# Kernel optimization log

Measured on AMD Instinct MI355X. Metric: run time of the kernel, lower is better.

Reference implementation:

```python
import jax, jax.numpy as jnp
from jax import lax
import numpy as np

PAD = 1          # padding (pair, symmetric)
STRIDE = (1, 1)  # (strideY, strideX)
KH, KW = 3, 3
C_IN, C_OUT = 256, 512


def setup_inputs() -> dict:
    key = jax.random.key(0)
    k1, k2 = jax.random.split(key)
    x = jax.random.normal(k1, (1, C_IN, 256, 256), dtype=jnp.float32)
    # reset_parameters: uniform(-stdv, stdv), stdv = 1/sqrt(numel(weight))
    stdv = 1.0 / np.sqrt(C_OUT * C_IN * KH * KW)
    weight = jax.random.uniform(k2, (C_OUT, C_IN, KH, KW), dtype=jnp.float32,
                                minval=-stdv, maxval=stdv)
    return {"x": x, "weight": weight}


def reference(x, weight):
    # pad H and W with constant value 1 (as in module's pad())
    xp = jnp.pad(x, ((0, 0), (0, 0), (PAD, PAD), (PAD, PAD)), constant_values=1.0)
    # binarize input: (x >= 0) -> +1 else -1 (detached in torch; non-diff anyway)
    xb = jnp.where(xp >= 0, 1.0, -1.0).astype(x.dtype)
    # input_K: channel-mean of |x| then avg_pool2d(kernel, stride), VALID
    abs_mean = jnp.mean(jnp.abs(xp), axis=1)  # [B, Hp, Wp]
    k_sum = lax.reduce_window(abs_mean, 0.0, lax.add,
                              (1, KH, KW), (1,) + STRIDE, 'VALID')
    input_K = k_sum / (KH * KW)  # [B, Ho, Wo]
    # binary conv (real-valued emulation of XNOR+popcount)
    conv = lax.conv_general_dilated(xb, weight, window_strides=STRIDE,
                                    padding='VALID',
                                    dimension_numbers=('NCHW', 'OIHW', 'NCHW'))
    # weight_alpha: per-output-channel mean of weight (note: mean, not abs-mean,
    # in the training-path forward())
    alpha = jnp.mean(weight, axis=(1, 2, 3))  # [C_out]
    return conv * input_K[:, None, :, :] * alpha[None, :, None, None]
```

## Files before the change

kernel.cpp:

```cpp
#include <hip/hip_runtime.h>

typedef unsigned short UST;
typedef unsigned int u32;
typedef __attribute__((ext_vector_type(4))) int i32x4;

#define HPAD 258
#define CIN 256
#define COUT 512
#define KTOT 2304

#define SCALES_OFF (COUT * KTOT)
#define XBT_OFF    (SCALES_OFF + 2048)
#define XBT_BYTES  (HPAD * HPAD * CIN)
#define ABSM_OFF   (XBT_OFF + XBT_BYTES)
#define ABSM_BYTES (HPAD * HPAD * 4)
#define INK_OFF    (ABSM_OFF + ABSM_BYTES)

__device__ __forceinline__ void gload_lds16(const void* g, void* l) {
  __builtin_amdgcn_global_load_lds(
      (const __attribute__((address_space(1))) u32*)g,
      (__attribute__((address_space(3))) u32*)l, 16, 0, 0);
}

__global__ __launch_bounds__(256) void k_prep_w(const float* __restrict__ w,
                                                signed char* __restrict__ wq,
                                                float* __restrict__ scales) {
  int co = blockIdx.x;
  int ci = threadIdx.x;
  const float* wr = w + co * KTOT + ci * 9;
  float v[9];
  float s = 0.f, mx = 0.f;
#pragma unroll
  for (int j = 0; j < 9; ++j) {
    v[j] = wr[j]; s += v[j]; mx = fmaxf(mx, fabsf(v[j]));
  }
  __shared__ float redS[256];
  __shared__ float redM[256];
  redS[ci] = s; redM[ci] = mx;
  __syncthreads();
#pragma unroll
  for (int off = 128; off > 0; off >>= 1) {
    if (ci < off) {
      redS[ci] += redS[ci + off];
      redM[ci] = fmaxf(redM[ci], redM[ci + off]);
    }
    __syncthreads();
  }
  float alpha = redS[0] * (1.0f / 2304.0f);
  float maxw = redM[0];
  float inv = 127.0f / maxw;
  signed char* wo = wq + co * KTOT + ci;
#pragma unroll
  for (int j = 0; j < 9; ++j)
    wo[j * 256] = (signed char)__float2int_rn(v[j] * inv);
  if (ci == 0) scales[co] = alpha * maxw * (1.0f / 127.0f);
}

__global__ __launch_bounds__(256) void k_binz(const float* __restrict__ x,
                                              signed char* __restrict__ xbt,
                                              float* __restrict__ absm) {
  int hp = blockIdx.x;
  int wt = blockIdx.y;
  int wpl = threadIdx.x & 63;
  int chunk = threadIdx.x >> 6;
  int wp = wt * 64 + wpl;
  bool valid = wp < HPAD;
  int hx = hp - 1, wx = wp - 1;
  bool inb = valid && ((unsigned)hx < 256u) && ((unsigned)wx < 256u);
  float asum = 0.f;
  u32 pk[16];
#pragma unroll
  for (int c4 = 0; c4 < 16; ++c4) {
    u32 word = 0;
#pragma unroll
    for (int b = 0; b < 4; ++b) {
      int ci = chunk * 64 + c4 * 4 + b;
      float v = 1.0f;
      if (inb) v = x[(unsigned)ci * 65536u + (unsigned)(hx * 256 + wx)];
      asum += fabsf(v);
      u32 byte = (v >= 0.f) ? 0x01u : 0xFFu;
      word |= byte << (8 * b);
    }
    pk[c4] = word;
  }
  if (valid) {
    uint4* dst = (uint4*)(xbt + (unsigned)(hp * HPAD + wp) * 256u + chunk * 64);
#pragma unroll
    for (int g = 0; g < 4; ++g)
      dst[g] = make_uint4(pk[g * 4], pk[g * 4 + 1], pk[g * 4 + 2], pk[g * 4 + 3]);
  }
  __shared__ float red[4][64];
  red[chunk][wpl] = asum;
  __syncthreads();
  if (chunk == 0 && valid) {
    float tot = red[0][wpl] + red[1][wpl] + red[2][wpl] + red[3][wpl];
    absm[hp * HPAD + wp] = tot * (1.0f / 256.0f);
  }
}

__global__ __launch_bounds__(256) void k_inputk(const float* __restrict__ absm,
                                                float* __restrict__ inK) {
  int h = blockIdx.x, w = threadIdx.x;
  float s = 0.f;
#pragma unroll
  for (int dh = 0; dh < 3; ++dh)
#pragma unroll
    for (int dw = 0; dw < 3; ++dw) s += absm[(h + dh) * HPAD + (w + dw)];
  inK[h * 256 + w] = s * (1.0f / 9.0f);
}

#define MMI(a, b, c) __builtin_amdgcn_mfma_i32_16x16x64_i8(a, b, c, 0, 0, 0)

#define A_LDS(S) (lds + (S) * 32768)
#define B_LDS(S) (lds + 65536 + (S) * 32768)
#define RD_A(S, KS, M) (*(const i32x4*)(A_LDS(S) + swzA[KS][M]))
#define RD_B(S, KS, N) (*(const i32x4*)(B_LDS(S) + swzB[KS][N]))

#define STAGE_A(SRC, S) do { \
    char* d_ = A_LDS(S) + wv * 1024; \
    gload_lds16((SRC) + aoff[0], d_); \
    gload_lds16((SRC) + aoff[1], d_ + 8192); \
    gload_lds16((SRC) + aoff[2], d_ + 16384); \
    gload_lds16((SRC) + aoff[3], d_ + 24576); } while (0)

#define STAGE_B(SRC, S) do { \
    char* d_ = B_LDS(S) + wv * 1024; \
    gload_lds16((SRC) + boff[0], d_); \
    gload_lds16((SRC) + boff[1], d_ + 8192); \
    gload_lds16((SRC) + boff[2], d_ + 16384); \
    gload_lds16((SRC) + boff[3], d_ + 24576); } while (0)

#define SB __builtin_amdgcn_sched_barrier(0)
#define VMW(N) asm volatile("s_waitcnt vmcnt(" #N ")" ::: "memory")
#define LGK0 asm volatile("s_waitcnt lgkmcnt(0)" ::: "memory")

#define RDB4(S, KS, D) \
  D[0] = RD_B(S, KS, 0); D[1] = RD_B(S, KS, 1); \
  D[2] = RD_B(S, KS, 2); D[3] = RD_B(S, KS, 3);
#define RDALO(S, KS, D) \
  D[0] = RD_A(S, KS, 0); D[1] = RD_A(S, KS, 1); \
  D[2] = RD_A(S, KS, 2); D[3] = RD_A(S, KS, 3);
#define RDAHI(S, KS, D) \
  D[0] = RD_A(S, KS, 4); D[1] = RD_A(S, KS, 5); \
  D[2] = RD_A(S, KS, 6); D[3] = RD_A(S, KS, 7);

#define MF_LO(AA, BB) \
  __builtin_amdgcn_s_setprio(1); \
  _Pragma("unroll") for (int m = 0; m < 4; ++m) \
  _Pragma("unroll") for (int n = 0; n < 4; ++n) \
    acc[m][n] = MMI(AA[m], BB[n], acc[m][n]); \
  __builtin_amdgcn_s_setprio(0);
#define MF_HI(AA, BB) \
  __builtin_amdgcn_s_setprio(1); \
  _Pragma("unroll") for (int m = 0; m < 4; ++m) \
  _Pragma("unroll") for (int n = 0; n < 4; ++n) \
    acc[m + 4][n] = MMI(AA[m], BB[n], acc[m + 4][n]); \
  __builtin_amdgcn_s_setprio(0);

#define BGPX(TT) (xbt_b + ((h + ((TT) >> 1) / 3) * HPAD + (((TT) >> 1) % 3)) * 256 \
                  + ((TT) & 1) * 128)

#define BODY(CA, CB, SA, SBT, TA, TB, ASRC, BSRC) do { \
  i32x4 Ahi_[4], B1_[4], A1lo_[4], A1hi_[4]; \
  RDAHI(CA, 0, Ahi_); \
  STAGE_A((ASRC), SA); STAGE_B((BSRC), SBT); \
  SB; MF_LO(Alo_, B0_); SB; \
  RDB4(CB, 1, B1_); RDALO(CA, 1, A1lo_); \
  SB; MF_HI(Ahi_, B0_); SB; \
  RDAHI(CA, 1, A1hi_); \
  SB; MF_LO(A1lo_, B1_); SB; \
  LGK0; VMW(4); \
  __builtin_amdgcn_s_barrier(); \
  RDB4(TB, 0, B0_); RDALO(TA, 0, Alo_); \
  SB; MF_HI(A1hi_, B1_); SB; \
} while (0)

#define BU(U) BODY((U) & 1, (U) % 3, ((U) + 1) & 1, ((U) + 2) % 3, \
                   ((U) + 1) & 1, ((U) + 1) % 3, \
                   wb_b + ((U) + 1) * 128, BGPX((U) + 2))

#define BODY16() do { \
  i32x4 Ahi_[4], B1_[4], A1lo_[4], A1hi_[4]; \
  RDAHI(0, 0, Ahi_); \
  STAGE_A(wb_b + 17 * 128, 1); \
  SB; MF_LO(Alo_, B0_); SB; \
  RDB4(1, 1, B1_); RDALO(0, 1, A1lo_); \
  SB; MF_HI(Ahi_, B0_); SB; \
  RDAHI(0, 1, A1hi_); \
  SB; MF_LO(A1lo_, B1_); SB; \
  LGK0; VMW(0); \
  __builtin_amdgcn_s_barrier(); \
  RDB4(2, 0, B0_); RDALO(1, 0, Alo_); \
  SB; MF_HI(A1hi_, B1_); SB; \
} while (0)

#define BODY17() do { \
  i32x4 Ahi_[4], B1_[4], A1lo_[4], A1hi_[4]; \
  RDAHI(1, 0, Ahi_); \
  SB; MF_LO(Alo_, B0_); SB; \
  RDB4(2, 1, B1_); RDALO(1, 1, A1lo_); \
  SB; MF_HI(Ahi_, B0_); SB; \
  RDAHI(1, 1, A1hi_); \
  SB; MF_LO(A1lo_, B1_); SB; \
  SB; MF_HI(A1hi_, B1_); SB; \
} while (0)

__global__ __launch_bounds__(512, 1) void k_conv8(const signed char* __restrict__ wq,
                                                  const signed char* __restrict__ xbt,
                                                  const float* __restrict__ scales,
                                                  const float* __restrict__ inK,
                                                  float* __restrict__ out) {
  __shared__ __align__(16) char lds[163840];
  int tid = threadIdx.x;
  int lane = tid & 63;
  int wv = tid >> 6;
  int wm = wv >> 2, wn = wv & 3;
  int bid = blockIdx.x;
  int bs = (bid & 7) * 64 + (bid >> 3);
  int mt = bs & 1;
  int h = bs >> 1;
  int co0 = mt << 8;

  int aoff[4], boff[4];
#pragma unroll
  for (int i = 0; i < 4; ++i) {
    u32 ql = (u32)(i * 512 + tid) * 16u;
    u32 row = ql >> 7;
    u32 s = (ql >> 4) & 7u;
    u32 slot = s ^ (row & 7u);
    aoff[i] = (int)((co0 + row) * 2304u + slot * 16u);
    boff[i] = (int)(row * 256u + slot * 16u);
  }
  int swzA[2][8], swzB[2][4];
#pragma unroll
  for (int ks = 0; ks < 2; ++ks) {
#pragma unroll
    for (int m = 0; m < 8; ++m) {
      u32 row = (u32)(wm * 128 + m * 16 + (lane & 15));
      u32 slot = (u32)(ks * 4 + (lane >> 4));
      swzA[ks][m] = (int)(row * 128u + (slot ^ (row & 7u)) * 16u);
    }
#pragma unroll
    for (int n = 0; n < 4; ++n) {
      u32 row = (u32)(wn * 64 + n * 16 + (lane & 15));
      u32 slot = (u32)(ks * 4 + (lane >> 4));
      swzB[ks][n] = (int)(row * 128u + (slot ^ (row & 7u)) * 16u);
    }
  }

  const char* wb_b = (const char*)wq;
  const char* xbt_b = (const char*)xbt;

  i32x4 acc[8][4];
#pragma unroll
  for (int m = 0; m < 8; ++m)
#pragma unroll
    for (int n = 0; n < 4; ++n) acc[m][n] = (i32x4){0, 0, 0, 0};

  i32x4 B0_[4], Alo_[4];

  STAGE_A(wb_b, 0);
  STAGE_B(BGPX(0), 0);
  STAGE_B(BGPX(1), 1);
  VMW(4);
  __builtin_amdgcn_s_barrier();
  RDB4(0, 0, B0_); RDALO(0, 0, Alo_);

  BU(0); BU(1); BU(2); BU(3); BU(4); BU(5); BU(6); BU(7);
  BU(8); BU(9); BU(10); BU(11); BU(12); BU(13); BU(14); BU(15);
  BODY16();
  BODY17();

  int col = lane & 15, rg = lane >> 4;
  int pixbase = h * 256;
#pragma unroll
  for (int n = 0; n < 4; ++n) {
    int w = wn * 64 + n * 16 + col;
    float kv = inK[pixbase + w];
#pragma unroll
    for (int m = 0; m < 8; ++m) {
      int cobase = co0 + wm * 128 + m * 16 + rg * 4;
      float4 scv = *(const float4*)(scales + cobase);
      float* o = out + (u32)cobase * 65536u + (u32)(pixbase + w);
      o[0]           = (float)acc[m][n][0] * scv.x * kv;
      o[65536u]      = (float)acc[m][n][1] * scv.y * kv;
      o[2u * 65536u] = (float)acc[m][n][2] * scv.z * kv;
      o[3u * 65536u] = (float)acc[m][n][3] * scv.w * kv;
    }
  }
}

extern "C" void kernel_launch(void* const* d_in, const int* in_sizes, int n_in,
                              void* d_out, int out_size, void* d_ws, size_t ws_size,
                              hipStream_t stream) {
  const float* x = (const float*)d_in[0];
  const float* w = (const float*)d_in[1];
  float* out = (float*)d_out;
  char* ws = (char*)d_ws;
  signed char* wq = (signed char*)ws;
  float* scales = (float*)(ws + SCALES_OFF);
  signed char* xbt = (signed char*)(ws + XBT_OFF);
  float* absm = (float*)(ws + ABSM_OFF);
  float* inK = (float*)(ws + INK_OFF);

  k_prep_w<<<COUT, 256, 0, stream>>>(w, wq, scales);
  k_binz<<<dim3(HPAD, 5), 256, 0, stream>>>(x, xbt, absm);
  k_inputk<<<256, 256, 0, stream>>>(absm, inK);
  k_conv8<<<512, 512, 0, stream>>>(wq, xbt, scales, inK, out);
}
```

Before: 108.6 us.

## Merge prep kernels into one launch, fold inputK into conv epilogue, hoist Ahi reads

```diff
diff --git a/kernel.cpp b/kernel.cpp
--- a/kernel.cpp
+++ b/kernel.cpp
@@ -13,8 +13,6 @@
 #define XBT_OFF    (SCALES_OFF + 2048)
 #define XBT_BYTES  (HPAD * HPAD * CIN)
 #define ABSM_OFF   (XBT_OFF + XBT_BYTES)
-#define ABSM_BYTES (HPAD * HPAD * 4)
-#define INK_OFF    (ABSM_OFF + ABSM_BYTES)
 
 __device__ __forceinline__ void gload_lds16(const void* g, void* l) {
   __builtin_amdgcn_global_load_lds(
@@ -22,91 +20,83 @@
       (__attribute__((address_space(3))) u32*)l, 16, 0, 0);
 }
 
-__global__ __launch_bounds__(256) void k_prep_w(const float* __restrict__ w,
-                                                signed char* __restrict__ wq,
-                                                float* __restrict__ scales) {
-  int co = blockIdx.x;
-  int ci = threadIdx.x;
-  const float* wr = w + co * KTOT + ci * 9;
-  float v[9];
-  float s = 0.f, mx = 0.f;
-#pragma unroll
-  for (int j = 0; j < 9; ++j) {
-    v[j] = wr[j]; s += v[j]; mx = fmaxf(mx, fabsf(v[j]));
-  }
-  __shared__ float redS[256];
-  __shared__ float redM[256];
-  redS[ci] = s; redM[ci] = mx;
-  __syncthreads();
-#pragma unroll
-  for (int off = 128; off > 0; off >>= 1) {
-    if (ci < off) {
-      redS[ci] += redS[ci + off];
-      redM[ci] = fmaxf(redM[ci], redM[ci + off]);
-    }
-    __syncthreads();
-  }
-  float alpha = redS[0] * (1.0f / 2304.0f);
-  float maxw = redM[0];
-  float inv = 127.0f / maxw;
-  signed char* wo = wq + co * KTOT + ci;
-#pragma unroll
-  for (int j = 0; j < 9; ++j)
-    wo[j * 256] = (signed char)__float2int_rn(v[j] * inv);
-  if (ci == 0) scales[co] = alpha * maxw * (1.0f / 127.0f);
-}
-
-__global__ __launch_bounds__(256) void k_binz(const float* __restrict__ x,
+__global__ __launch_bounds__(256) void k_prep(const float* __restrict__ w,
+                                              signed char* __restrict__ wq,
+                                              float* __restrict__ scales,
+                                              const float* __restrict__ x,
                                               signed char* __restrict__ xbt,
                                               float* __restrict__ absm) {
-  int hp = blockIdx.x;
-  int wt = blockIdx.y;
-  int wpl = threadIdx.x & 63;
-  int chunk = threadIdx.x >> 6;
-  int wp = wt * 64 + wpl;
-  bool valid = wp < HPAD;
-  int hx = hp - 1, wx = wp - 1;
-  bool inb = valid && ((unsigned)hx < 256u) && ((unsigned)wx < 256u);
-  float asum = 0.f;
-  u32 pk[16];
-#pragma unroll
-  for (int c4 = 0; c4 < 16; ++c4) {
-    u32 word = 0;
-#pragma unroll
-    for (int b = 0; b < 4; ++b) {
-      int ci = chunk * 64 + c4 * 4 + b;
-      float v = 1.0f;
-      if (inb) v = x[(unsigned)ci * 65536u + (unsigned)(hx * 256 + wx)];
-      asum += fabsf(v);
-      u32 byte = (v >= 0.f) ? 0x01u : 0xFFu;
-      word |= byte << (8 * b);
-    }
-    pk[c4] = word;
-  }
-  if (valid) {
-    uint4* dst = (uint4*)(xbt + (unsigned)(hp * HPAD + wp) * 256u + chunk * 64);
-#pragma unroll
-    for (int g = 0; g < 4; ++g)
-      dst[g] = make_uint4(pk[g * 4], pk[g * 4 + 1], pk[g * 4 + 2], pk[g * 4 + 3]);
-  }
-  __shared__ float red[4][64];
-  red[chunk][wpl] = asum;
-  __syncthreads();
-  if (chunk == 0 && valid) {
-    float tot = red[0][wpl] + red[1][wpl] + red[2][wpl] + red[3][wpl];
-    absm[hp * HPAD + wp] = tot * (1.0f / 256.0f);
-  }
-}
-
-__global__ __launch_bounds__(256) void k_inputk(const float* __restrict__ absm,
-                                                float* __restrict__ inK) {
-  int h = blockIdx.x, w = threadIdx.x;
-  float s = 0.f;
-#pragma unroll
-  for (int dh = 0; dh < 3; ++dh)
-#pragma unroll
-    for (int dw = 0; dw < 3; ++dw) s += absm[(h + dh) * HPAD + (w + dw)];
-  inK[h * 256 + w] = s * (1.0f / 9.0f);
+  int bid = blockIdx.x;
+  if (bid < COUT) {
+    int co = bid;
+    int ci = threadIdx.x;
+    const float* wr = w + co * KTOT + ci * 9;
+    float v[9];
+    float s = 0.f, mx = 0.f;
+#pragma unroll
+    for (int j = 0; j < 9; ++j) {
+      v[j] = wr[j]; s += v[j]; mx = fmaxf(mx, fabsf(v[j]));
+    }
+    __shared__ float redS[256];
+    __shared__ float redM[256];
+    redS[ci] = s; redM[ci] = mx;
+    __syncthreads();
+#pragma unroll
+    for (int off = 128; off > 0; off >>= 1) {
+      if (ci < off) {
+        redS[ci] += redS[ci + off];
+        redM[ci] = fmaxf(redM[ci], redM[ci + off]);
+      }
+      __syncthreads();
+    }
+    float alpha = redS[0] * (1.0f / 2304.0f);
+    float maxw = redM[0];
+    float inv = 127.0f / maxw;
+    signed char* wo = wq + co * KTOT + ci;
+#pragma unroll
+    for (int j = 0; j < 9; ++j)
+      wo[j * 256] = (signed char)__float2int_rn(v[j] * inv);
+    if (ci == 0) scales[co] = alpha * maxw * (1.0f / 127.0f);
+  } else {
+    int b2 = bid - COUT;
+    int hp = b2 / 5;
+    int wt = b2 - hp * 5;
+    int wpl = threadIdx.x & 63;
+    int chunk = threadIdx.x >> 6;
+    int wp = wt * 64 + wpl;
+    bool valid = wp < HPAD;
+    int hx = hp - 1, wx = wp - 1;
+    bool inb = valid && ((unsigned)hx < 256u) && ((unsigned)wx < 256u);
+    float asum = 0.f;
+    u32 pk[16];
+#pragma unroll
+    for (int c4 = 0; c4 < 16; ++c4) {
+      u32 word = 0;
+#pragma unroll
+      for (int b = 0; b < 4; ++b) {
+        int ci = chunk * 64 + c4 * 4 + b;
+        float v = 1.0f;
+        if (inb) v = x[(unsigned)ci * 65536u + (unsigned)(hx * 256 + wx)];
+        asum += fabsf(v);
+        u32 byte = (v >= 0.f) ? 0x01u : 0xFFu;
+        word |= byte << (8 * b);
+      }
+      pk[c4] = word;
+    }
+    if (valid) {
+      uint4* dst = (uint4*)(xbt + (unsigned)(hp * HPAD + wp) * 256u + chunk * 64);
+#pragma unroll
+      for (int g = 0; g < 4; ++g)
+        dst[g] = make_uint4(pk[g * 4], pk[g * 4 + 1], pk[g * 4 + 2], pk[g * 4 + 3]);
+    }
+    __shared__ float red[4][64];
+    red[chunk][wpl] = asum;
+    __syncthreads();
+    if (chunk == 0 && valid) {
+      float tot = red[0][wpl] + red[1][wpl] + red[2][wpl] + red[3][wpl];
+      absm[hp * HPAD + wp] = tot * (1.0f / 256.0f);
+    }
+  }
 }
 
 #define MMI(a, b, c) __builtin_amdgcn_mfma_i32_16x16x64_i8(a, b, c, 0, 0, 0)
@@ -161,8 +151,7 @@
                   + ((TT) & 1) * 128)
 
 #define BODY(CA, CB, SA, SBT, TA, TB, ASRC, BSRC) do { \
-  i32x4 Ahi_[4], B1_[4], A1lo_[4], A1hi_[4]; \
-  RDAHI(CA, 0, Ahi_); \
+  i32x4 B1_[4], A1lo_[4], A1hi_[4]; \
   STAGE_A((ASRC), SA); STAGE_B((BSRC), SBT); \
   SB; MF_LO(Alo_, B0_); SB; \
   RDB4(CB, 1, B1_); RDALO(CA, 1, A1lo_); \
@@ -171,7 +160,7 @@
   SB; MF_LO(A1lo_, B1_); SB; \
   LGK0; VMW(4); \
   __builtin_amdgcn_s_barrier(); \
-  RDB4(TB, 0, B0_); RDALO(TA, 0, Alo_); \
+  RDB4(TB, 0, B0_); RDALO(TA, 0, Alo_); RDAHI(TA, 0, Ahi_); \
   SB; MF_HI(A1hi_, B1_); SB; \
 } while (0)
 
@@ -180,8 +169,7 @@
                    wb_b + ((U) + 1) * 128, BGPX((U) + 2))
 
 #define BODY16() do { \
-  i32x4 Ahi_[4], B1_[4], A1lo_[4], A1hi_[4]; \
-  RDAHI(0, 0, Ahi_); \
+  i32x4 B1_[4], A1lo_[4], A1hi_[4]; \
   STAGE_A(wb_b + 17 * 128, 1); \
   SB; MF_LO(Alo_, B0_); SB; \
   RDB4(1, 1, B1_); RDALO(0, 1, A1lo_); \
@@ -190,13 +178,12 @@
   SB; MF_LO(A1lo_, B1_); SB; \
   LGK0; VMW(0); \
   __builtin_amdgcn_s_barrier(); \
-  RDB4(2, 0, B0_); RDALO(1, 0, Alo_); \
+  RDB4(2, 0, B0_); RDALO(1, 0, Alo_); RDAHI(1, 0, Ahi_); \
   SB; MF_HI(A1hi_, B1_); SB; \
 } while (0)
 
 #define BODY17() do { \
-  i32x4 Ahi_[4], B1_[4], A1lo_[4], A1hi_[4]; \
-  RDAHI(1, 0, Ahi_); \
+  i32x4 B1_[4], A1lo_[4], A1hi_[4]; \
   SB; MF_LO(Alo_, B0_); SB; \
   RDB4(2, 1, B1_); RDALO(1, 1, A1lo_); \
   SB; MF_HI(Ahi_, B0_); SB; \
@@ -208,7 +195,7 @@
 __global__ __launch_bounds__(512, 1) void k_conv8(const signed char* __restrict__ wq,
                                                   const signed char* __restrict__ xbt,
                                                   const float* __restrict__ scales,
-                                                  const float* __restrict__ inK,
+                                                  const float* __restrict__ absm,
                                                   float* __restrict__ out) {
   __shared__ __align__(16) char lds[163840];
   int tid = threadIdx.x;
@@ -257,14 +244,14 @@
 #pragma unroll
     for (int n = 0; n < 4; ++n) acc[m][n] = (i32x4){0, 0, 0, 0};
 
-  i32x4 B0_[4], Alo_[4];
+  i32x4 B0_[4], Alo_[4], Ahi_[4];
 
   STAGE_A(wb_b, 0);
   STAGE_B(BGPX(0), 0);
   STAGE_B(BGPX(1), 1);
   VMW(4);
   __builtin_amdgcn_s_barrier();
-  RDB4(0, 0, B0_); RDALO(0, 0, Alo_);
+  RDB4(0, 0, B0_); RDALO(0, 0, Alo_); RDAHI(0, 0, Ahi_);
 
   BU(0); BU(1); BU(2); BU(3); BU(4); BU(5); BU(6); BU(7);
   BU(8); BU(9); BU(10); BU(11); BU(12); BU(13); BU(14); BU(15);
@@ -273,10 +260,22 @@
 
   int col = lane & 15, rg = lane >> 4;
   int pixbase = h * 256;
+  float kvv[4];
 #pragma unroll
   for (int n = 0; n < 4; ++n) {
     int w = wn * 64 + n * 16 + col;
-    float kv = inK[pixbase + w];
+    float s = 0.f;
+#pragma unroll
+    for (int dh = 0; dh < 3; ++dh)
+#pragma unroll
+      for (int dw = 0; dw < 3; ++dw)
+        s += absm[(h + dh) * HPAD + (w + dw)];
+    kvv[n] = s * (1.0f / 9.0f);
+  }
+#pragma unroll
+  for (int n = 0; n < 4; ++n) {
+    int w = wn * 64 + n * 16 + col;
+    float kv = kvv[n];
 #pragma unroll
     for (int m = 0; m < 8; ++m) {
       int cobase = co0 + wm * 128 + m * 16 + rg * 4;
@@ -301,10 +300,7 @@
   float* scales = (float*)(ws + SCALES_OFF);
   signed char* xbt = (signed char*)(ws + XBT_OFF);
   float* absm = (float*)(ws + ABSM_OFF);
-  float* inK = (float*)(ws + INK_OFF);
-
-  k_prep_w<<<COUT, 256, 0, stream>>>(w, wq, scales);
-  k_binz<<<dim3(HPAD, 5), 256, 0, stream>>>(x, xbt, absm);
-  k_inputk<<<256, 256, 0, stream>>>(absm, inK);
-  k_conv8<<<512, 512, 0, stream>>>(wq, xbt, scales, inK, out);
+
+  k_prep<<<COUT + HPAD * 5, 256, 0, stream>>>(w, wq, scales, x, xbt, absm);
+  k_conv8<<<512, 512, 0, stream>>>(wq, xbt, scales, absm, out);
 }
```

Measured after the change: 110.3 us. No clear change (+1.6%).
